# Optimization experiments

Hardware: AMD Instinct MI355X
Metric: run time of the kernel (lower is better)

## Reference

```python
import jax, jax.numpy as jnp
import numpy as np

B, N, HID, H = 2, 2048, 2048, 16
DH = HID // H  # 128


def _rope_tables(n, d, base=10000.0):
    inv_freq = 1.0 / (base ** (np.arange(0, d, 2, dtype=np.float32) / d))
    t = np.arange(n, dtype=np.float32)
    freqs = np.outer(t, inv_freq)                 # [N, d/2]
    emb = np.concatenate([freqs, freqs], axis=-1)  # [N, d]
    return jnp.asarray(np.cos(emb)), jnp.asarray(np.sin(emb))


def setup_inputs() -> dict:
    key = jax.random.key(0)
    k1, k2, k3 = jax.random.split(key, 3)
    std = 1.0 / HID ** 0.5
    cos, sin = _rope_tables(N, DH)
    return {
        "hidden_states": jax.random.normal(k1, (B, N, HID), dtype=jnp.float32),
        "cos": cos,
        "sin": sin,
        "w_qkv": (jax.random.truncated_normal(k2, -2.0, 2.0, (3 * HID, HID), jnp.float32) * std),
        "w_o": (jax.random.truncated_normal(k3, -2.0, 2.0, (HID, HID), jnp.float32) * std),
    }


def _rotate_half(x):
    d = x.shape[-1] // 2
    return jnp.concatenate([-x[..., d:], x[..., :d]], axis=-1)


def reference(hidden_states, cos, sin, w_qkv, w_o):
    b, n, _ = hidden_states.shape
    qkv = (hidden_states @ w_qkv.T).reshape(b, n, 3, H, DH)
    q, k, v = qkv[:, :, 0], qkv[:, :, 1], qkv[:, :, 2]  # [B,N,H,DH]
    c = cos[:, None, :]  # [N,1,DH] broadcasts over heads
    s = sin[:, None, :]
    q = q * c + _rotate_half(q) * s
    k = k * c + _rotate_half(k) * s
    scale = 1.0 / jnp.sqrt(jnp.asarray(DH, q.dtype))
    scores = jnp.einsum("bqhd,bkhd->bhqk", q, k) * scale
    attn = jax.nn.softmax(scores, axis=-1)
    out = jnp.einsum("bhqk,bkhd->bqhd", attn, v).reshape(b, n, HID)
    return out @ w_o.T
```

## Files before the change

### kernel.cpp

```cpp
#include <hip/hip_runtime.h>
#include <math.h>

#define NB 2
#define NN 2048
#define HIDDEN 2048
#define NHEAD 16
#define DHEAD 128

typedef __attribute__((ext_vector_type(8))) short bf16x8;
typedef __attribute__((ext_vector_type(4))) float floatx4;

static __device__ __forceinline__ short f2bf(float f) {
    union { float f; unsigned u; } v; v.f = f;
    unsigned r = v.u + 0x7fffu + ((v.u >> 16) & 1u);
    return (short)(r >> 16);
}
static __device__ __forceinline__ void gload_lds16(const short* g, short* l) {
    __builtin_amdgcn_global_load_lds(
        (const __attribute__((address_space(1))) void*)g,
        (__attribute__((address_space(3))) void*)l, 16, 0, 0);
}

__global__ __launch_bounds__(256) void cast_bf16_3(
    const float* __restrict__ a, const float* __restrict__ b, const float* __restrict__ c,
    short* __restrict__ oa, short* __restrict__ ob, short* __restrict__ oc,
    int n4a, int n4b, int n4c)
{
    int i = blockIdx.x * 256 + threadIdx.x;
    const float* s; short* d; int j;
    if (i < n4a) { s = a; d = oa; j = i; }
    else if (i < n4a + n4b) { s = b; d = ob; j = i - n4a; }
    else if (i < n4a + n4b + n4c) { s = c; d = oc; j = i - n4a - n4b; }
    else return;
    float4 v = ((const float4*)s)[j];
    short4 o;
    o.x = f2bf(v.x); o.y = f2bf(v.y); o.z = f2bf(v.z); o.w = f2bf(v.w);
    ((short4*)d)[j] = o;
}

template <int MODE>
__global__ __launch_bounds__(256) void gemm_bf16_nt(
    const short* __restrict__ A, const short* __restrict__ Bw,
    const float* __restrict__ cosT, const float* __restrict__ sinT,
    short* __restrict__ Qp, short* __restrict__ Kp, short* __restrict__ Vtp,
    float* __restrict__ Cp, int M, int N, int K)
{
    __shared__ __align__(16) short AB[1280 * 8];

    const int tid = threadIdx.x;
    const int w = tid >> 6;
    const int l = tid & 63;
    const int quad = l >> 4;
    const int l15 = l & 15;
    const int bm = blockIdx.y * 128;
    const int bn = blockIdx.x * 128;

    const int wm = (w & 1) * 64;
    const int wn2 = w >> 1;

    const short* gptr[5];
    short* lptr[5];
#pragma unroll
    for (int r5 = 0; r5 < 5; ++r5) {
        int s = r5 * 256 + tid;
        int m = (s < 640) ? s : s - 640;
        int row = m / 5;
        int ch = m - row * 5;
        if (ch == 4) ch = 0;
        gptr[r5] = ((s < 640) ? (A + (size_t)(bm + row) * K)
                              : (Bw + (size_t)(bn + row) * K)) + ch * 8;
        lptr[r5] = &AB[s * 8];
    }

    floatx4 acc[4][4];
#pragma unroll
    for (int i = 0; i < 4; ++i)
#pragma unroll
        for (int j = 0; j < 4; ++j) acc[i][j] = (floatx4){0.f, 0.f, 0.f, 0.f};

    for (int k0 = 0; k0 < K; k0 += 32) {
        __syncthreads();
#pragma unroll
        for (int r5 = 0; r5 < 5; ++r5)
            gload_lds16(gptr[r5] + k0, lptr[r5]);
        __syncthreads();

        bf16x8 af[4], bf[4];
#pragma unroll
        for (int i = 0; i < 4; ++i)
            af[i] = *(const bf16x8*)&AB[((wm + i * 16 + l15) * 5 + quad) * 8];
#pragma unroll
        for (int j = 0; j < 4; ++j) {
            int col = wn2 * 32 + (j & 1) * 16 + ((j >> 1) << 6);
            bf[j] = *(const bf16x8*)&AB[(640 + (col + l15) * 5 + quad) * 8];
        }
#pragma unroll
        for (int i = 0; i < 4; ++i)
#pragma unroll
            for (int j = 0; j < 4; ++j)
                acc[i][j] = __builtin_amdgcn_mfma_f32_16x16x32_bf16(af[i], bf[j], acc[i][j], 0, 0, 0);
    }

    if (MODE == 1) {
#pragma unroll
        for (int i = 0; i < 4; ++i) {
#pragma unroll
            for (int reg = 0; reg < 4; ++reg) {
                int row = bm + wm + i * 16 + quad * 4 + reg;
                float* crow = Cp + (size_t)row * N + bn;
#pragma unroll
                for (int j = 0; j < 4; ++j)
                    crow[wn2 * 32 + (j & 1) * 16 + ((j >> 1) << 6) + l15] = acc[i][j][reg];
            }
        }
    } else {
        const int which = bn >> 11;
        const int head = (bn >> 7) & (NHEAD - 1);
        const float qsc = (which == 0) ? 0.12751791525f : 1.0f;
#pragma unroll
        for (int i = 0; i < 4; ++i) {
#pragma unroll
            for (int reg = 0; reg < 4; ++reg) {
                int m = bm + wm + i * 16 + quad * 4 + reg;
                int b = m >> 11, n = m & (NN - 1);
                int bh = b * NHEAD + head;
                if (which == 2) {
#pragma unroll
                    for (int j = 0; j < 4; ++j) {
                        int d = wn2 * 32 + (j & 1) * 16 + ((j >> 1) << 6) + l15;
                        Vtp[((size_t)bh * DHEAD + d) * NN + n] = f2bf(acc[i][j][reg]);
                    }
                } else {
                    short* dst = (which == 0 ? Qp : Kp) + ((size_t)bh * NN + n) * DHEAD;
#pragma unroll
                    for (int j = 0; j < 2; ++j) {
                        int d0 = wn2 * 32 + j * 16 + l15;
                        float c = cosT[(size_t)n * DHEAD + d0];
                        float s = sinT[(size_t)n * DHEAD + d0];
                        float e0 = acc[i][j][reg], e1 = acc[i][j + 2][reg];
                        dst[d0]      = f2bf((e0 * c - e1 * s) * qsc);
                        dst[d0 + 64] = f2bf((e1 * c + e0 * s) * qsc);
                    }
                }
            }
        }
    }
}

__global__ __launch_bounds__(256, 2) void attn_mfma(
    const short* __restrict__ Qb, const short* __restrict__ Kb,
    const short* __restrict__ Vt, short* __restrict__ AOb)
{
    __shared__ __align__(16) short Ks[64 * 128];
    __shared__ __align__(16) short Vs[128 * 64];
    __shared__ __align__(16) short Ps[4][32][72];

    const int tid = threadIdx.x;
    const int w = tid >> 6;
    const int l = tid & 63;
    const int quad = l >> 4;
    const int l15 = l & 15;
    const int bh = blockIdx.y;
    const int qt = blockIdx.x * 128;

    const short* Qg = Qb + (size_t)bh * NN * DHEAD;
    const short* Kg = Kb + (size_t)bh * NN * DHEAD;
    const short* Vg = Vt + (size_t)bh * DHEAD * NN;

    bf16x8 qf[2][4];
#pragma unroll
    for (int mi = 0; mi < 2; ++mi) {
        const short* qrow = Qg + (size_t)(qt + w * 32 + mi * 16 + l15) * DHEAD + quad * 8;
#pragma unroll
        for (int kc = 0; kc < 4; ++kc) qf[mi][kc] = *(const bf16x8*)(qrow + kc * 32);
    }

    floatx4 of[2][8];
#pragma unroll
    for (int mi = 0; mi < 2; ++mi)
#pragma unroll
        for (int dc = 0; dc < 8; ++dc) of[mi][dc] = (floatx4){0.f, 0.f, 0.f, 0.f};
    float ls[2][4] = {{0.f, 0.f, 0.f, 0.f}, {0.f, 0.f, 0.f, 0.f}};

    for (int kt = 0; kt < NN; kt += 64) {
        __syncthreads();
#pragma unroll
        for (int rr = 0; rr < 4; ++rr) {
            int s = (w * 4 + rr) * 64 + l;
            int row = s >> 4;
            int j = (s & 15) ^ (row & 15);
            gload_lds16(Kg + (size_t)(kt + row) * DHEAD + j * 8, &Ks[s * 8]);
        }
#pragma unroll
        for (int rr = 0; rr < 4; ++rr) {
            int s = (w * 4 + rr) * 64 + l;
            int row = s >> 3;
            int c = (s & 7) ^ (row & 7);
            gload_lds16(Vg + (size_t)row * NN + kt + c * 8, &Vs[s * 8]);
        }
        __syncthreads();

        floatx4 sf[2][4];
#pragma unroll
        for (int n16 = 0; n16 < 4; ++n16) {
            bf16x8 kf[4];
            const short* kbase = &Ks[(n16 * 16 + l15) * 128];
#pragma unroll
            for (int kc = 0; kc < 4; ++kc)
                kf[kc] = *(const bf16x8*)&kbase[((4 * kc + quad) ^ l15) * 8];
#pragma unroll
            for (int mi = 0; mi < 2; ++mi) {
                floatx4 acc = (floatx4){0.f, 0.f, 0.f, 0.f};
#pragma unroll
                for (int kc = 0; kc < 4; ++kc)
                    acc = __builtin_amdgcn_mfma_f32_16x16x32_bf16(qf[mi][kc], kf[kc], acc, 0, 0, 0);
                sf[mi][n16] = acc;
            }
        }

#pragma unroll
        for (int mi = 0; mi < 2; ++mi)
#pragma unroll
            for (int n16 = 0; n16 < 4; ++n16)
#pragma unroll
                for (int r = 0; r < 4; ++r) {
                    float p = exp2f(sf[mi][n16][r]);
                    ls[mi][r] += p;
                    Ps[w][mi * 16 + quad * 4 + r][n16 * 16 + l15] = f2bf(p);
                }

        bf16x8 pa[2][2];
#pragma unroll
        for (int mi = 0; mi < 2; ++mi)
#pragma unroll
            for (int kc = 0; kc < 2; ++kc)
                pa[mi][kc] = *(const bf16x8*)&Ps[w][mi * 16 + l15][kc * 32 + quad * 8];

#pragma unroll
        for (int dc = 0; dc < 8; ++dc) {
            int row = dc * 16 + l15;
#pragma unroll
            for (int kc = 0; kc < 2; ++kc) {
                bf16x8 vf = *(const bf16x8*)&Vs[row * 64 + (((kc * 4 + quad) ^ (row & 7)) * 8)];
#pragma unroll
                for (int mi = 0; mi < 2; ++mi)
                    of[mi][dc] = __builtin_amdgcn_mfma_f32_16x16x32_bf16(
                                     pa[mi][kc], vf, of[mi][dc], 0, 0, 0);
            }
        }
    }

    const int b = bh >> 4, h = bh & (NHEAD - 1);
#pragma unroll
    for (int mi = 0; mi < 2; ++mi)
#pragma unroll
        for (int r = 0; r < 4; ++r) {
            float s = ls[mi][r];
            s += __shfl_xor(s, 1, 64);
            s += __shfl_xor(s, 2, 64);
            s += __shfl_xor(s, 4, 64);
            s += __shfl_xor(s, 8, 64);
            float inv = 1.0f / s;
            int row = qt + w * 32 + mi * 16 + quad * 4 + r;
            short* dst = AOb + ((size_t)(b * NN + row)) * HIDDEN + h * DHEAD;
#pragma unroll
            for (int dc = 0; dc < 8; ++dc)
                dst[dc * 16 + l15] = f2bf(of[mi][dc][r] * inv);
        }
}

extern "C" void kernel_launch(void* const* d_in, const int* in_sizes, int n_in,
                              void* d_out, int out_size, void* d_ws, size_t ws_size,
                              hipStream_t stream)
{
    const float* hs = (const float*)d_in[0];
    const float* cosT = (const float*)d_in[1];
    const float* sinT = (const float*)d_in[2];
    const float* wqkv = (const float*)d_in[3];
    const float* wo = (const float*)d_in[4];
    float* out = (float*)d_out;

    const size_t N_HS = (size_t)NB * NN * HIDDEN;
    const size_t N_WQ = (size_t)3 * HIDDEN * HIDDEN;
    const size_t N_WO = (size_t)HIDDEN * HIDDEN;
    const size_t SZ = (size_t)NB * NHEAD * NN * DHEAD;

    short* Ahs   = (short*)d_ws;
    short* Wqkvb = Ahs + N_HS;
    short* Wob   = Wqkvb + N_WQ;
    short* Qb    = Wob + N_WO;
    short* Kb    = Qb + SZ;
    short* Vtb   = Kb + SZ;
    short* AOb   = Vtb + SZ;

    {
        int n4a = (int)(N_HS / 4), n4b = (int)(N_WQ / 4), n4c = (int)(N_WO / 4);
        int total = n4a + n4b + n4c;
        cast_bf16_3<<<(total + 255) / 256, 256, 0, stream>>>(
            hs, wqkv, wo, Ahs, Wqkvb, Wob, n4a, n4b, n4c);
    }
    {
        dim3 grid(3 * HIDDEN / 128, NB * NN / 128);
        gemm_bf16_nt<0><<<grid, 256, 0, stream>>>(
            Ahs, Wqkvb, cosT, sinT, Qb, Kb, Vtb, nullptr,
            NB * NN, 3 * HIDDEN, HIDDEN);
    }
    {
        dim3 grid(NN / 128, NB * NHEAD);
        attn_mfma<<<grid, 256, 0, stream>>>(Qb, Kb, Vtb, AOb);
    }
    {
        dim3 grid(HIDDEN / 128, NB * NN / 128);
        gemm_bf16_nt<1><<<grid, 256, 0, stream>>>(
            AOb, Wob, nullptr, nullptr, nullptr, nullptr, nullptr, out,
            NB * NN, HIDDEN, HIDDEN);
    }
}
```

Before: 466.1 us.

## Add 256x256 tiled QKV GEMM with double-buffered LDS and interleaved MFMA

Replaces the 128x128 QKV projection GEMM with a new 512-thread kernel that computes 256x256 tiles. It uses a 128KB double-buffered LDS staged through global_load_lds, with prefetch interleaved between four MFMA phases and barriers. The RoPE, Q-scale and V-transpose epilogue is rewritten to suit the new tile mapping. Larger tiles increase operand reuse and cut global traffic, but the grid shrinks to 24x16 blocks, which raises register and LDS pressure and lowers occupancy.

Result: faster. 428.1 us (-8.2%).

```diff
diff --git a/kernel.cpp b/kernel.cpp
--- a/kernel.cpp
+++ b/kernel.cpp
@@ -38,6 +38,183 @@
     ((short4*)d)[j] = o;
 }
 
+__global__ __launch_bounds__(512, 2) void gemm_qkv_256(
+    const short* __restrict__ A, const short* __restrict__ Bw,
+    const float* __restrict__ cosT, const float* __restrict__ sinT,
+    short* __restrict__ Qp, short* __restrict__ Kp, short* __restrict__ Vtp)
+{
+    __shared__ __align__(16) short AB[65536];
+
+    const int tid = threadIdx.x;
+    const int w = tid >> 6;
+    const int l = tid & 63;
+    const int quad = l >> 4;
+    const int l15 = l & 15;
+    const int wr = w >> 2;
+    const int wc = w & 3;
+    const int bm = blockIdx.y * 256;
+    const int bn = blockIdx.x * 256;
+    const int K = HIDDEN;
+
+    const short* src[8];
+    int ldst[8];
+#pragma unroll
+    for (int ld = 0; ld < 2; ++ld) {
+        int chunk = ld * 512 + tid;
+        int row = chunk >> 3;
+        int j = (chunk & 7) ^ (row & 7);
+        int coff = j * 8;
+        int dbase = chunk * 16;
+        src[0 * 2 + ld] = Bw + (size_t)(bn + row) * K + coff;
+        src[1 * 2 + ld] = A  + (size_t)(bm + row) * K + coff;
+        src[2 * 2 + ld] = A  + (size_t)(bm + 128 + row) * K + coff;
+        src[3 * 2 + ld] = Bw + (size_t)(bn + 128 + row) * K + coff;
+        ldst[0 * 2 + ld] = 32768 + dbase;
+        ldst[1 * 2 + ld] = 0 + dbase;
+        ldst[2 * 2 + ld] = 16384 + dbase;
+        ldst[3 * 2 + ld] = 32768 + 16384 + dbase;
+    }
+
+    const int xj = l15 & 7;
+    const int jq0 = ((0 * 4 + quad) ^ xj) * 16;
+    const int jq1 = ((1 * 4 + quad) ^ xj) * 16;
+    const int arow = (wr * 128 + l15) * 128;
+    const int brow = (wc * 16 + l15) * 128;
+
+    floatx4 acc[8][4];
+#pragma unroll
+    for (int i = 0; i < 8; ++i)
+#pragma unroll
+        for (int j = 0; j < 4; ++j) acc[i][j] = (floatx4){0.f, 0.f, 0.f, 0.f};
+
+#pragma unroll
+    for (int i = 0; i < 8; ++i)
+        gload_lds16(src[i], (short*)((char*)AB + ldst[i]));
+
+#define STAGE(i) gload_lds16(src[i] + kpf, (short*)((char*)AB + ldst[i] + so))
+#define MFMA(d, x, y) d = __builtin_amdgcn_mfma_f32_16x16x32_bf16(x, y, d, 0, 0, 0)
+
+    const int NT = K / 64;
+#pragma unroll 1
+    for (int t = 0; t < NT; ++t) {
+        const int co = (t & 1) << 16;
+        const int so = co ^ 65536;
+        int kpf = (t + 1) * 64;
+        if (kpf == K) kpf = 0;
+
+        bf16x8 a[4][2], b0[2][2], b1[2][2];
+
+        asm volatile("s_waitcnt vmcnt(2)" ::: "memory");
+        __builtin_amdgcn_s_barrier();
+#pragma unroll
+        for (int m = 0; m < 4; ++m) {
+            a[m][0] = *(const bf16x8*)((const char*)AB + co + arow + m * 2048 + jq0);
+            a[m][1] = *(const bf16x8*)((const char*)AB + co + arow + m * 2048 + jq1);
+        }
+#pragma unroll
+        for (int n = 0; n < 2; ++n) {
+            b0[n][0] = *(const bf16x8*)((const char*)AB + co + 32768 + brow + n * 8192 + jq0);
+            b0[n][1] = *(const bf16x8*)((const char*)AB + co + 32768 + brow + n * 8192 + jq1);
+        }
+        STAGE(0); STAGE(1);
+        __builtin_amdgcn_s_setprio(1);
+#pragma unroll
+        for (int m = 0; m < 4; ++m)
+#pragma unroll
+            for (int n = 0; n < 2; ++n) {
+                MFMA(acc[m][n], a[m][0], b0[n][0]);
+                MFMA(acc[m][n], a[m][1], b0[n][1]);
+            }
+        __builtin_amdgcn_s_setprio(0);
+
+        asm volatile("s_waitcnt vmcnt(2)" ::: "memory");
+        __builtin_amdgcn_s_barrier();
+#pragma unroll
+        for (int n = 0; n < 2; ++n) {
+            b1[n][0] = *(const bf16x8*)((const char*)AB + co + 32768 + 16384 + brow + n * 8192 + jq0);
+            b1[n][1] = *(const bf16x8*)((const char*)AB + co + 32768 + 16384 + brow + n * 8192 + jq1);
+        }
+        STAGE(2); STAGE(3);
+        __builtin_amdgcn_s_setprio(1);
+#pragma unroll
+        for (int m = 0; m < 4; ++m)
+#pragma unroll
+            for (int n = 0; n < 2; ++n) {
+                MFMA(acc[m][2 + n], a[m][0], b1[n][0]);
+                MFMA(acc[m][2 + n], a[m][1], b1[n][1]);
+            }
+        __builtin_amdgcn_s_setprio(0);
+
+        __builtin_amdgcn_s_barrier();
+#pragma unroll
+        for (int m = 0; m < 4; ++m) {
+            a[m][0] = *(const bf16x8*)((const char*)AB + co + arow + (4 + m) * 2048 + jq0);
+            a[m][1] = *(const bf16x8*)((const char*)AB + co + arow + (4 + m) * 2048 + jq1);
+        }
+        STAGE(4); STAGE(5);
+        __builtin_amdgcn_s_setprio(1);
+#pragma unroll
+        for (int m = 0; m < 4; ++m)
+#pragma unroll
+            for (int n = 0; n < 2; ++n) {
+                MFMA(acc[4 + m][2 + n], a[m][0], b1[n][0]);
+                MFMA(acc[4 + m][2 + n], a[m][1], b1[n][1]);
+            }
+        __builtin_amdgcn_s_setprio(0);
+
+        __builtin_amdgcn_s_barrier();
+        STAGE(6); STAGE(7);
+        __builtin_amdgcn_s_setprio(1);
+#pragma unroll
+        for (int m = 0; m < 4; ++m)
+#pragma unroll
+            for (int n = 0; n < 2; ++n) {
+                MFMA(acc[4 + m][n], a[m][0], b0[n][0]);
+                MFMA(acc[4 + m][n], a[m][1], b0[n][1]);
+            }
+        __builtin_amdgcn_s_setprio(0);
+    }
+#undef STAGE
+#undef MFMA
+
+    asm volatile("s_waitcnt vmcnt(0)" ::: "memory");
+
+    const int bx = blockIdx.x;
+    const int which = bx >> 3;
+    const int hpair = (bx & 7) * 2;
+    const float qsc = (which == 0) ? 0.12751791525f : 1.0f;
+
+#pragma unroll
+    for (int m = 0; m < 8; ++m) {
+#pragma unroll
+        for (int reg = 0; reg < 4; ++reg) {
+            int gm = bm + wr * 128 + m * 16 + quad * 4 + reg;
+            int b = gm >> 11, nseq = gm & (NN - 1);
+            if (which == 2) {
+#pragma unroll
+                for (int n = 0; n < 4; ++n) {
+                    int bh = b * NHEAD + hpair + (n >> 1);
+                    int d = (n & 1) * 64 + wc * 16 + l15;
+                    Vtp[((size_t)bh * DHEAD + d) * NN + nseq] = f2bf(acc[m][n][reg]);
+                }
+            } else {
+                int d0 = wc * 16 + l15;
+                float c = cosT[(size_t)nseq * DHEAD + d0];
+                float s = sinT[(size_t)nseq * DHEAD + d0];
+#pragma unroll
+                for (int hb = 0; hb < 2; ++hb) {
+                    int bh = b * NHEAD + hpair + hb;
+                    short* dst = (which == 0 ? Qp : Kp) + ((size_t)bh * NN + nseq) * DHEAD;
+                    float e0 = acc[m][hb * 2 + 0][reg];
+                    float e1 = acc[m][hb * 2 + 1][reg];
+                    dst[d0]      = f2bf((e0 * c - e1 * s) * qsc);
+                    dst[d0 + 64] = f2bf((e1 * c + e0 * s) * qsc);
+                }
+            }
+        }
+    }
+}
+
 template <int MODE>
 __global__ __launch_bounds__(256) void gemm_bf16_nt(
     const short* __restrict__ A, const short* __restrict__ Bw,
@@ -300,10 +477,9 @@
             hs, wqkv, wo, Ahs, Wqkvb, Wob, n4a, n4b, n4c);
     }
     {
-        dim3 grid(3 * HIDDEN / 128, NB * NN / 128);
-        gemm_bf16_nt<0><<<grid, 256, 0, stream>>>(
-            Ahs, Wqkvb, cosT, sinT, Qb, Kb, Vtb, nullptr,
-            NB * NN, 3 * HIDDEN, HIDDEN);
+        dim3 grid(3 * HIDDEN / 256, NB * NN / 256);
+        gemm_qkv_256<<<grid, 512, 0, stream>>>(
+            Ahs, Wqkvb, cosT, sinT, Qb, Kb, Vtb);
     }
     {
         dim3 grid(NN / 128, NB * NHEAD);
```

## Add 256x128 QKV GEMM kernel with 512 threads and split-phase prefetch

Applied to the files above, without the earlier changes.

Replaces the 128x128 QKV projection GEMM with a dedicated 256x128-tile kernel using 8 waves and a double-buffered LDS of 96KB. Global-to-LDS loads go through an XOR-swizzled layout and are issued in two phases interleaved with MFMA groups, raising MFMA priority with s_setprio. The RoPE, Q-scaling and V-transpose epilogue is kept. The goal is more operand reuse per tile and better overlap of loads with compute, at the cost of heavy LDS use that limits occupancy to about one block per CU.

Measured after the change: 433.9 us. -6.9%, faster.

```diff
diff --git a/kernel.cpp b/kernel.cpp
--- a/kernel.cpp
+++ b/kernel.cpp
@@ -38,6 +38,154 @@
     ((short4*)d)[j] = o;
 }
 
+__global__ __launch_bounds__(512, 2) void gemm_qkv_256x128(
+    const short* __restrict__ A, const short* __restrict__ Bw,
+    const float* __restrict__ cosT, const float* __restrict__ sinT,
+    short* __restrict__ Qp, short* __restrict__ Kp, short* __restrict__ Vtp)
+{
+    __shared__ __align__(16) short AB[49152];
+
+    const int tid = threadIdx.x;
+    const int w = tid >> 6;
+    const int l = tid & 63;
+    const int quad = l >> 4;
+    const int l15 = l & 15;
+    const int bn = blockIdx.x * 128;
+    const int bm = blockIdx.y * 256;
+    const int K = HIDDEN;
+
+    const short* src[6];
+    int ldst[6];
+#pragma unroll
+    for (int ld = 0; ld < 2; ++ld) {
+        int chunk = ld * 512 + tid;
+        int row = chunk >> 3;
+        int j = (chunk & 7) ^ (row & 7);
+        int coff = j * 8;
+        src[ld]     = A + (size_t)(bm + row) * K + coff;
+        src[2 + ld] = A + (size_t)(bm + 128 + row) * K + coff;
+        ldst[ld]     = chunk * 16;
+        ldst[2 + ld] = 16384 + chunk * 16;
+    }
+    {
+        int row = tid >> 3;
+        int j = (tid & 7) ^ (row & 7);
+        int coff = j * 8;
+        src[4] = Bw + (size_t)(bn + row) * K + coff;
+        src[5] = Bw + (size_t)(bn + 64 + row) * K + coff;
+        ldst[4] = 32768 + tid * 16;
+        ldst[5] = 32768 + 8192 + tid * 16;
+    }
+
+    const int xj = l15 & 7;
+    const int jq0 = ((0 * 4 + quad) ^ xj) * 16;
+    const int jq1 = ((1 * 4 + quad) ^ xj) * 16;
+    const int arow = (w * 32 + l15) * 128;
+    const int brow = 32768 + l15 * 128;
+
+    floatx4 acc[2][8];
+#pragma unroll
+    for (int i = 0; i < 2; ++i)
+#pragma unroll
+        for (int j = 0; j < 8; ++j) acc[i][j] = (floatx4){0.f, 0.f, 0.f, 0.f};
+
+#pragma unroll
+    for (int i = 0; i < 6; ++i)
+        gload_lds16(src[i], (short*)((char*)AB + ldst[i]));
+
+#define STAGE(i) gload_lds16(src[i] + kpf, (short*)((char*)AB + ldst[i] + so))
+#define MFMA(d, x, y) d = __builtin_amdgcn_mfma_f32_16x16x32_bf16(x, y, d, 0, 0, 0)
+
+    const int NT = K / 64;
+#pragma unroll 1
+    for (int t = 0; t < NT; ++t) {
+        const int co = (t & 1) * 49152;
+        const int so = co ^ 49152;
+        int kpf = (t + 1) * 64;
+        if (kpf == K) kpf = 0;
+
+        bf16x8 a[2][2], b[4][2];
+
+        asm volatile("s_waitcnt vmcnt(1)" ::: "memory");
+        __builtin_amdgcn_s_barrier();
+#pragma unroll
+        for (int m = 0; m < 2; ++m) {
+            a[m][0] = *(const bf16x8*)((const char*)AB + co + arow + m * 2048 + jq0);
+            a[m][1] = *(const bf16x8*)((const char*)AB + co + arow + m * 2048 + jq1);
+        }
+#pragma unroll
+        for (int n = 0; n < 4; ++n) {
+            b[n][0] = *(const bf16x8*)((const char*)AB + co + brow + n * 2048 + jq0);
+            b[n][1] = *(const bf16x8*)((const char*)AB + co + brow + n * 2048 + jq1);
+        }
+        STAGE(0); STAGE(1); STAGE(2); STAGE(3); STAGE(4);
+        __builtin_amdgcn_s_setprio(1);
+#pragma unroll
+        for (int m = 0; m < 2; ++m)
+#pragma unroll
+            for (int n = 0; n < 4; ++n) {
+                MFMA(acc[m][n], a[m][0], b[n][0]);
+                MFMA(acc[m][n], a[m][1], b[n][1]);
+            }
+        __builtin_amdgcn_s_setprio(0);
+
+        asm volatile("s_waitcnt vmcnt(5)" ::: "memory");
+        __builtin_amdgcn_s_barrier();
+#pragma unroll
+        for (int n = 0; n < 4; ++n) {
+            b[n][0] = *(const bf16x8*)((const char*)AB + co + brow + (4 + n) * 2048 + jq0);
+            b[n][1] = *(const bf16x8*)((const char*)AB + co + brow + (4 + n) * 2048 + jq1);
+        }
+        STAGE(5);
+        __builtin_amdgcn_s_setprio(1);
+#pragma unroll
+        for (int m = 0; m < 2; ++m)
+#pragma unroll
+            for (int n = 0; n < 4; ++n) {
+                MFMA(acc[m][4 + n], a[m][0], b[n][0]);
+                MFMA(acc[m][4 + n], a[m][1], b[n][1]);
+            }
+        __builtin_amdgcn_s_setprio(0);
+    }
+#undef STAGE
+#undef MFMA
+
+    asm volatile("s_waitcnt vmcnt(0)" ::: "memory");
+
+    const int which = bn >> 11;
+    const int head = (bn >> 7) & (NHEAD - 1);
+    const float qsc = (which == 0) ? 0.12751791525f : 1.0f;
+
+#pragma unroll
+    for (int m = 0; m < 2; ++m) {
+#pragma unroll
+        for (int reg = 0; reg < 4; ++reg) {
+            int gm = bm + w * 32 + m * 16 + quad * 4 + reg;
+            int b2 = gm >> 11, nseq = gm & (NN - 1);
+            int bh = b2 * NHEAD + head;
+            if (which == 2) {
+#pragma unroll
+                for (int n = 0; n < 8; ++n) {
+                    int d = n * 16 + l15;
+                    Vtp[((size_t)bh * DHEAD + d) * NN + nseq] = f2bf(acc[m][n][reg]);
+                }
+            } else {
+                short* dst = (which == 0 ? Qp : Kp) + ((size_t)bh * NN + nseq) * DHEAD;
+#pragma unroll
+                for (int p = 0; p < 4; ++p) {
+                    int d0 = p * 16 + l15;
+                    float c = cosT[(size_t)nseq * DHEAD + d0];
+                    float s = sinT[(size_t)nseq * DHEAD + d0];
+                    float e0 = acc[m][p][reg];
+                    float e1 = acc[m][p + 4][reg];
+                    dst[d0]      = f2bf((e0 * c - e1 * s) * qsc);
+                    dst[d0 + 64] = f2bf((e1 * c + e0 * s) * qsc);
+                }
+            }
+        }
+    }
+}
+
 template <int MODE>
 __global__ __launch_bounds__(256) void gemm_bf16_nt(
     const short* __restrict__ A, const short* __restrict__ Bw,
@@ -300,10 +448,9 @@
             hs, wqkv, wo, Ahs, Wqkvb, Wob, n4a, n4b, n4c);
     }
     {
-        dim3 grid(3 * HIDDEN / 128, NB * NN / 128);
-        gemm_bf16_nt<0><<<grid, 256, 0, stream>>>(
-            Ahs, Wqkvb, cosT, sinT, Qb, Kb, Vtb, nullptr,
-            NB * NN, 3 * HIDDEN, HIDDEN);
+        dim3 grid(3 * HIDDEN / 128, NB * NN / 256);
+        gemm_qkv_256x128<<<grid, 512, 0, stream>>>(
+            Ahs, Wqkvb, cosT, sinT, Qb, Kb, Vtb);
     }
     {
         dim3 grid(NN / 128, NB * NHEAD);
```
